# Kernel tuning notes

Hardware: AMD Instinct MI355X
Metric: run time of the kernel (lower is better)

Reference implementation:

```python
import jax, jax.numpy as jnp
import numpy as np


def setup_inputs() -> dict:
    key = jax.random.key(0)
    k1, k2 = jax.random.split(key)
    B, N, M = 4, 8192, 8192
    xyz1 = jax.random.normal(k1, (B, N, 3), dtype=jnp.float32)
    xyz2 = jax.random.normal(k2, (B, M, 3), dtype=jnp.float32)
    th = jnp.float32(0.1)
    return {"xyz1": xyz1, "xyz2": xyz2, "th": th}


def reference(xyz1, xyz2, th):
    # Pairwise squared distances (B, N, M) via the expanded form
    x2 = jnp.sum(xyz1 * xyz1, axis=-1)                    # (B, N)
    y2 = jnp.sum(xyz2 * xyz2, axis=-1)                    # (B, M)
    cross = jnp.einsum('bnd,bmd->bnm', xyz1, xyz2)        # (B, N, M)
    dist = x2[:, :, None] + y2[:, None, :] - 2.0 * cross  # (B, N, M)
    # torch: distances is (B, M, N); min over dim=1 -> per-x min (our axis=2),
    #        min over dim=2 -> per-y min (our axis=1).
    d1 = jnp.min(dist, axis=2)                            # (B, N)
    d2 = jnp.min(dist, axis=1)                            # (B, M)
    d1 = jnp.where(d1 <= th, jnp.float32(0.0), d1)
    d2 = jnp.where(d2 <= th, jnp.float32(0.0), d2)
    return jnp.mean(d1, axis=1) + jnp.mean(d2, axis=1)    # (B,)
```

## Files before the change

kernel.cpp:

```cpp
#include <hip/hip_runtime.h>
#include <math.h>

#define NPTS 8192
#define LOSCALE 2048.0f
#define INVLO   (1.0f / 2048.0f)

typedef _Float16 half8  __attribute__((ext_vector_type(8)));
typedef float    f32x16 __attribute__((ext_vector_type(16)));

__device__ __forceinline__ float min3a(float m, float a, float b) {
    float r;
    asm("v_min3_f32 %0, %1, %2, %3" : "=v"(r) : "v"(m), "v"(a), "v"(b));
    return r;
}


__global__ __launch_bounds__(256) void prep_bfrag(
    const float* __restrict__ xyz1,
    const float* __restrict__ xyz2,
    half8* __restrict__ bfrag)
{
    const int gid  = blockIdx.x * 256 + threadIdx.x;
    const int col  = gid & 31;
    const int tile = (gid >> 5) & 255;
    const int c    = gid >> 13;
    const int s    = c >> 2, bb = c & 3;
    const float* src = (s == 0 ? xyz1 : xyz2)
                     + ((size_t)bb * NPTS + tile * 32 + col) * 3;
    const float px = src[0], py = src[1], pz = src[2];
    const _Float16 phx = (_Float16)px, phy = (_Float16)py, phz = (_Float16)pz;
    const _Float16 plx = (_Float16)((px - (float)phx) * LOSCALE);
    const _Float16 ply = (_Float16)((py - (float)phy) * LOSCALE);
    const _Float16 plz = (_Float16)((pz - (float)phz) * LOSCALE);
    const float pn = px * px + py * py + pz * pz;
    const _Float16 pnh = (_Float16)pn;
    const _Float16 pnl = (_Float16)((pn - (float)pnh) * LOSCALE);
    const _Float16 one = (_Float16)1.0f, z = (_Float16)0.0f;
    half8 hi = (half8){phx, phy, phz, one, pnh, z, z, z};
    half8 lo = (half8){phx, phy, phz, plx, ply, plz, one, pnl};
    half8* dst = bfrag + ((size_t)(c * 256 + tile) * 2) * 32 + col;
    dst[0]  = hi;
    dst[32] = lo;
}

__global__ __launch_bounds__(512, 2) void chamfer_mfma(
    const float* __restrict__ xyz1,
    const float* __restrict__ xyz2,
    const half8* __restrict__ bfrag,
    const float* __restrict__ thp,
    double* __restrict__ partial)
{
    __shared__ float  red[8][4][32];
    __shared__ double wsum[8];

    const int bid    = blockIdx.x;
    const int qchunk = bid & 31;
    const int combo  = bid >> 5;
    const int b      = combo & 3;
    const int dir    = combo >> 2;
    const float* Q   = (dir == 0 ? xyz1 : xyz2) + (size_t)b * NPTS * 3;
    const int   cref = (dir == 0 ? 4 : 0) + b;

    const int lane = threadIdx.x & 63;
    const int w    = threadIdx.x >> 6;
    const int h    = lane >> 5;
    const int col  = lane & 31;
    const int qg   = w >> 2;
    const int pq   = w & 3;

    const _Float16 one = (_Float16)1.0f, z16 = (_Float16)0.0f;
    const half8 zfrag = (half8){z16, z16, z16, z16, z16, z16, z16, z16};

    half8 Ah[4], Al[4];
    f32x16 m[4];
    #pragma unroll
    for (int lt = 0; lt < 4; ++lt) {
        const float* qp = Q + ((size_t)qchunk * 256 + (qg * 4 + lt) * 32 + col) * 3;
        const float qx = qp[0], qy = qp[1], qz = qp[2];
        const float ax = -2.0f * qx, ay = -2.0f * qy, az = -2.0f * qz;
        const _Float16 ahx = (_Float16)ax, ahy = (_Float16)ay, ahz = (_Float16)az;
        const _Float16 alx = (_Float16)((ax - (float)ahx) * LOSCALE);
        const _Float16 aly = (_Float16)((ay - (float)ahy) * LOSCALE);
        const _Float16 alz = (_Float16)((az - (float)ahz) * LOSCALE);
        const float qn = qx * qx + qy * qy + qz * qz;
        const _Float16 qnh = (_Float16)qn;
        const _Float16 qnl = (_Float16)((qn - (float)qnh) * LOSCALE);
        if (h == 0) {
            Ah[lt] = (half8){ahx, ahy, ahz, qnh, one, z16, z16, z16};
            Al[lt] = (half8){alx, aly, alz, ahx, ahy, ahz, qnl, one};
        } else {
            Ah[lt] = zfrag;
            Al[lt] = zfrag;
        }
        #pragma unroll
        for (int i = 0; i < 16; ++i) m[lt][i] = INFINITY;
    }

    f32x16 zc;
    #pragma unroll
    for (int i = 0; i < 16; ++i) zc[i] = 0.0f;

    const half8* bf = bfrag + (size_t)cref * 256 * 2 * 32 + col;
    const int t0 = pq * 64;

    half8 Bh0 = zfrag, Bl0 = zfrag, Bh1 = zfrag, Bl1 = zfrag;
    if (h == 0) {
        Bh0 = bf[((size_t)(t0 + 0) * 2 + 0) * 32];
        Bl0 = bf[((size_t)(t0 + 0) * 2 + 1) * 32];
        Bh1 = bf[((size_t)(t0 + 1) * 2 + 0) * 32];
        Bl1 = bf[((size_t)(t0 + 1) * 2 + 1) * 32];
    }

    #pragma unroll 1
    for (int jp = 0; jp < 32; ++jp) {
        half8 nh0 = Bh0, nl0 = Bl0, nh1 = Bh1, nl1 = Bl1;
        if (jp < 31 && h == 0) {
            const int tn = t0 + 2 * jp + 2;
            nh0 = bf[((size_t)(tn + 0) * 2 + 0) * 32];
            nl0 = bf[((size_t)(tn + 0) * 2 + 1) * 32];
            nh1 = bf[((size_t)(tn + 1) * 2 + 0) * 32];
            nl1 = bf[((size_t)(tn + 1) * 2 + 1) * 32];
        }
        #pragma unroll
        for (int lt = 0; lt < 4; ++lt) {
            f32x16 D1 = __builtin_amdgcn_mfma_f32_32x32x16_f16(Ah[lt], Bh0, zc, 0, 0, 0);
            f32x16 D2 = __builtin_amdgcn_mfma_f32_32x32x16_f16(Al[lt], Bl0, zc, 0, 0, 0);
            f32x16 E1 = __builtin_amdgcn_mfma_f32_32x32x16_f16(Ah[lt], Bh1, zc, 0, 0, 0);
            f32x16 E2 = __builtin_amdgcn_mfma_f32_32x32x16_f16(Al[lt], Bl1, zc, 0, 0, 0);
            #pragma unroll
            for (int i = 0; i < 16; ++i) {
                const float dA = fmaf(D2[i], INVLO, D1[i]);
                const float dB = fmaf(E2[i], INVLO, E1[i]);
                m[lt][i] = min3a(m[lt][i], dA, dB);
            }
        }
        Bh0 = nh0; Bl0 = nl0; Bh1 = nh1; Bl1 = nl1;
    }

    #pragma unroll
    for (int lt = 0; lt < 4; ++lt) {
        #pragma unroll
        for (int i = 0; i < 16; ++i) {
            float v = m[lt][i];
            v = fminf(v, __shfl_xor(v, 1, 64));
            v = fminf(v, __shfl_xor(v, 2, 64));
            v = fminf(v, __shfl_xor(v, 4, 64));
            v = fminf(v, __shfl_xor(v, 8, 64));
            v = fminf(v, __shfl_xor(v, 16, 64));
            m[lt][i] = v;
        }
    }
    if (col == 0) {
        #pragma unroll
        for (int lt = 0; lt < 4; ++lt)
            #pragma unroll
            for (int i = 0; i < 16; ++i)
                red[w][lt][(i & 3) + 8 * (i >> 2) + 4 * h] = m[lt][i];
    }
    __syncthreads();

    double val = 0.0;
    if (threadIdx.x < 256) {
        const int gt  = threadIdx.x >> 5;
        const int r   = threadIdx.x & 31;
        const int qg2 = gt >> 2, lt = gt & 3;
        float mv =            red[qg2 * 4 + 0][lt][r];
        mv = fminf(mv, red[qg2 * 4 + 1][lt][r]);
        mv = fminf(mv, red[qg2 * 4 + 2][lt][r]);
        mv = fminf(mv, red[qg2 * 4 + 3][lt][r]);
        val = (mv <= *thp) ? 0.0 : (double)mv;
    }
    for (int off = 32; off > 0; off >>= 1)
        val += __shfl_down(val, off, 64);
    if (lane == 0) wsum[w] = val;
    __syncthreads();
    if (threadIdx.x == 0) {
        double s = 0.0;
        #pragma unroll
        for (int i = 0; i < 8; ++i) s += wsum[i];
        partial[bid] = s;
    }
}

__global__ __launch_bounds__(256) void chamfer_fin(
    const double* __restrict__ partial,
    float* __restrict__ out)
{
    const int b = threadIdx.x >> 6;
    const int l = threadIdx.x & 63;
    double v = (l < 32) ? partial[b * 32 + l]
                        : partial[(4 + b) * 32 + (l - 32)];
    for (int off = 32; off > 0; off >>= 1)
        v += __shfl_down(v, off, 64);
    if (l == 0) out[b] = (float)(v / (double)NPTS);
}

extern "C" void kernel_launch(void* const* d_in, const int* in_sizes, int n_in,
                              void* d_out, int out_size, void* d_ws, size_t ws_size,
                              hipStream_t stream) {
    const float* xyz1 = (const float*)d_in[0];
    const float* xyz2 = (const float*)d_in[1];
    const float* thp  = (const float*)d_in[2];
    float* out        = (float*)d_out;

    half8*  bfrag   = (half8*)d_ws;
    double* partial = (double*)((char*)d_ws + (size_t)8 * 256 * 2 * 32 * 16);

    prep_bfrag<<<256, 256, 0, stream>>>(xyz1, xyz2, bfrag);
    chamfer_mfma<<<256, 512, 0, stream>>>(xyz1, xyz2, bfrag, thp, partial);
    chamfer_fin<<<1, 256, 0, stream>>>(partial, out);
}
```

Before: 51.19 us.

## Chain hi/lo split MFMAs into accumulating pair and re-split work across blocks

Repacks the fp16 hi/lo split so the correction terms ride in the unused upper K slots of the first fragment, then chains the two MFMAs through the accumulator instead of computing two separate products and combining them with FMAs. This removes the per-element fmaf combine step from the inner loop. Work is redistributed to 512 blocks of 128 queries, with each wave scanning 32 reference tiles instead of 64. The fragments now fill both halves of the wave, so loads are unconditional, and the prep buffer doubles in size. The 64x scale factor changes the rounding behaviour of the split and may affect precision.

```diff
diff --git a/kernel.cpp b/kernel.cpp
--- a/kernel.cpp
+++ b/kernel.cpp
@@ -2,8 +2,6 @@
 #include <math.h>
 
 #define NPTS 8192
-#define LOSCALE 2048.0f
-#define INVLO   (1.0f / 2048.0f)
 
 typedef _Float16 half8  __attribute__((ext_vector_type(8)));
 typedef float    f32x16 __attribute__((ext_vector_type(16)));
@@ -21,26 +19,35 @@
     half8* __restrict__ bfrag)
 {
     const int gid  = blockIdx.x * 256 + threadIdx.x;
-    const int col  = gid & 31;
-    const int tile = (gid >> 5) & 255;
-    const int c    = gid >> 13;
+    const int lane = gid & 63;
+    const int tile = (gid >> 6) & 255;
+    const int c    = gid >> 14;
     const int s    = c >> 2, bb = c & 3;
-    const float* src = (s == 0 ? xyz1 : xyz2)
-                     + ((size_t)bb * NPTS + tile * 32 + col) * 3;
-    const float px = src[0], py = src[1], pz = src[2];
-    const _Float16 phx = (_Float16)px, phy = (_Float16)py, phz = (_Float16)pz;
-    const _Float16 plx = (_Float16)((px - (float)phx) * LOSCALE);
-    const _Float16 ply = (_Float16)((py - (float)phy) * LOSCALE);
-    const _Float16 plz = (_Float16)((pz - (float)phz) * LOSCALE);
-    const float pn = px * px + py * py + pz * pz;
-    const _Float16 pnh = (_Float16)pn;
-    const _Float16 pnl = (_Float16)((pn - (float)pnh) * LOSCALE);
-    const _Float16 one = (_Float16)1.0f, z = (_Float16)0.0f;
-    half8 hi = (half8){phx, phy, phz, one, pnh, z, z, z};
-    half8 lo = (half8){phx, phy, phz, plx, ply, plz, one, pnl};
-    half8* dst = bfrag + ((size_t)(c * 256 + tile) * 2) * 32 + col;
-    dst[0]  = hi;
-    dst[32] = lo;
+    const int col  = lane & 31, h = lane >> 5;
+
+    half8 B1 = {}, B2 = {};
+    if (h == 0) {
+        const float* src = (s == 0 ? xyz1 : xyz2)
+                         + ((size_t)bb * NPTS + tile * 32 + col) * 3;
+        const float px = src[0], py = src[1], pz = src[2];
+        const _Float16 phx = (_Float16)px, phy = (_Float16)py, phz = (_Float16)pz;
+        const _Float16 pl64x = (_Float16)((px - (float)phx) * 64.0f);
+        const _Float16 pl64y = (_Float16)((py - (float)phy) * 64.0f);
+        const _Float16 pl64z = (_Float16)((pz - (float)phz) * 64.0f);
+        const _Float16 ph64x = (_Float16)((float)phx * (1.0f / 64.0f));
+        const _Float16 ph64y = (_Float16)((float)phy * (1.0f / 64.0f));
+        const _Float16 ph64z = (_Float16)((float)phz * (1.0f / 64.0f));
+        const float pn = px * px + py * py + pz * pz;
+        const _Float16 pnh = (_Float16)pn;
+        const _Float16 pnl64 = (_Float16)((pn - (float)pnh) * 64.0f);
+        const _Float16 one = (_Float16)1.0f, i64 = (_Float16)(1.0f / 64.0f);
+        const _Float16 z = (_Float16)0.0f;
+        B1 = (half8){phx, phy, phz, one, pnh, ph64x, ph64y, ph64z};
+        B2 = (half8){pl64x, pl64y, pl64z, i64, pnl64, z, z, z};
+    }
+    half8* dst = bfrag + ((size_t)(c * 256 + tile) * 2) * 64 + lane;
+    dst[0]  = B1;
+    dst[64] = B2;
 }
 
 __global__ __launch_bounds__(512, 2) void chamfer_mfma(
@@ -54,8 +61,8 @@
     __shared__ double wsum[8];
 
     const int bid    = blockIdx.x;
-    const int qchunk = bid & 31;
-    const int combo  = bid >> 5;
+    const int qchunk = bid & 63;
+    const int combo  = bid >> 6;
     const int b      = combo & 3;
     const int dir    = combo >> 2;
     const float* Q   = (dir == 0 ? xyz1 : xyz2) + (size_t)b * NPTS * 3;
@@ -65,32 +72,31 @@
     const int w    = threadIdx.x >> 6;
     const int h    = lane >> 5;
     const int col  = lane & 31;
-    const int qg   = w >> 2;
-    const int pq   = w & 3;
-
-    const _Float16 one = (_Float16)1.0f, z16 = (_Float16)0.0f;
-    const half8 zfrag = (half8){z16, z16, z16, z16, z16, z16, z16, z16};
-
-    half8 Ah[4], Al[4];
+
+    half8 A1[4], A2[4];
     f32x16 m[4];
     #pragma unroll
     for (int lt = 0; lt < 4; ++lt) {
-        const float* qp = Q + ((size_t)qchunk * 256 + (qg * 4 + lt) * 32 + col) * 3;
-        const float qx = qp[0], qy = qp[1], qz = qp[2];
-        const float ax = -2.0f * qx, ay = -2.0f * qy, az = -2.0f * qz;
-        const _Float16 ahx = (_Float16)ax, ahy = (_Float16)ay, ahz = (_Float16)az;
-        const _Float16 alx = (_Float16)((ax - (float)ahx) * LOSCALE);
-        const _Float16 aly = (_Float16)((ay - (float)ahy) * LOSCALE);
-        const _Float16 alz = (_Float16)((az - (float)ahz) * LOSCALE);
-        const float qn = qx * qx + qy * qy + qz * qz;
-        const _Float16 qnh = (_Float16)qn;
-        const _Float16 qnl = (_Float16)((qn - (float)qnh) * LOSCALE);
+        A1[lt] = (half8){};
+        A2[lt] = (half8){};
         if (h == 0) {
-            Ah[lt] = (half8){ahx, ahy, ahz, qnh, one, z16, z16, z16};
-            Al[lt] = (half8){alx, aly, alz, ahx, ahy, ahz, qnl, one};
-        } else {
-            Ah[lt] = zfrag;
-            Al[lt] = zfrag;
+            const float* qp = Q + ((size_t)qchunk * 128 + lt * 32 + col) * 3;
+            const float qx = qp[0], qy = qp[1], qz = qp[2];
+            const float ax = -2.0f * qx, ay = -2.0f * qy, az = -2.0f * qz;
+            const _Float16 ahx = (_Float16)ax, ahy = (_Float16)ay, ahz = (_Float16)az;
+            const _Float16 al64x = (_Float16)((ax - (float)ahx) * 64.0f);
+            const _Float16 al64y = (_Float16)((ay - (float)ahy) * 64.0f);
+            const _Float16 al64z = (_Float16)((az - (float)ahz) * 64.0f);
+            const _Float16 ah64x = (_Float16)((float)ahx * (1.0f / 64.0f));
+            const _Float16 ah64y = (_Float16)((float)ahy * (1.0f / 64.0f));
+            const _Float16 ah64z = (_Float16)((float)ahz * (1.0f / 64.0f));
+            const float qn = qx * qx + qy * qy + qz * qz;
+            const _Float16 qnh = (_Float16)qn;
+            const _Float16 qnl64 = (_Float16)((qn - (float)qnh) * 64.0f);
+            const _Float16 one = (_Float16)1.0f, i64 = (_Float16)(1.0f / 64.0f);
+            const _Float16 z16 = (_Float16)0.0f;
+            A1[lt] = (half8){ahx, ahy, ahz, qnh, one, al64x, al64y, al64z};
+            A2[lt] = (half8){ah64x, ah64y, ah64z, qnl64, i64, z16, z16, z16};
         }
         #pragma unroll
         for (int i = 0; i < 16; ++i) m[lt][i] = INFINITY;
@@ -100,42 +106,30 @@
     #pragma unroll
     for (int i = 0; i < 16; ++i) zc[i] = 0.0f;
 
-    const half8* bf = bfrag + (size_t)cref * 256 * 2 * 32 + col;
-    const int t0 = pq * 64;
-
-    half8 Bh0 = zfrag, Bl0 = zfrag, Bh1 = zfrag, Bl1 = zfrag;
-    if (h == 0) {
-        Bh0 = bf[((size_t)(t0 + 0) * 2 + 0) * 32];
-        Bl0 = bf[((size_t)(t0 + 0) * 2 + 1) * 32];
-        Bh1 = bf[((size_t)(t0 + 1) * 2 + 0) * 32];
-        Bl1 = bf[((size_t)(t0 + 1) * 2 + 1) * 32];
-    }
-
+    const half8* bf = bfrag + (size_t)cref * (256 * 2 * 64) + lane;
+    const int t0 = w * 32;
+
+#define LD(t, f) bf[(size_t)(((t0 + ((t) & 31)) * 2 + (f))) * 64]
+
+    half8 h0 = LD(0, 0), l0 = LD(0, 1);
+    half8 h1 = LD(1, 0), l1 = LD(1, 1);
     #pragma unroll 1
-    for (int jp = 0; jp < 32; ++jp) {
-        half8 nh0 = Bh0, nl0 = Bl0, nh1 = Bh1, nl1 = Bl1;
-        if (jp < 31 && h == 0) {
-            const int tn = t0 + 2 * jp + 2;
-            nh0 = bf[((size_t)(tn + 0) * 2 + 0) * 32];
-            nl0 = bf[((size_t)(tn + 0) * 2 + 1) * 32];
-            nh1 = bf[((size_t)(tn + 1) * 2 + 0) * 32];
-            nl1 = bf[((size_t)(tn + 1) * 2 + 1) * 32];
+    for (int jp = 0; jp < 16; ++jp) {
+        half8 nh0 = LD(2 * jp + 2, 0), nl0 = LD(2 * jp + 2, 1);
+        half8 nh1 = LD(2 * jp + 3, 0), nl1 = LD(2 * jp + 3, 1);
+        #pragma unroll
+        for (int lt = 0; lt < 4; ++lt) {
+            f32x16 D = __builtin_amdgcn_mfma_f32_32x32x16_f16(A1[lt], h0, zc, 0, 0, 0);
+            D = __builtin_amdgcn_mfma_f32_32x32x16_f16(A2[lt], l0, D, 0, 0, 0);
+            f32x16 E = __builtin_amdgcn_mfma_f32_32x32x16_f16(A1[lt], h1, zc, 0, 0, 0);
+            E = __builtin_amdgcn_mfma_f32_32x32x16_f16(A2[lt], l1, E, 0, 0, 0);
+            #pragma unroll
+            for (int i = 0; i < 16; ++i)
+                m[lt][i] = min3a(m[lt][i], D[i], E[i]);
         }
-        #pragma unroll
-        for (int lt = 0; lt < 4; ++lt) {
-            f32x16 D1 = __builtin_amdgcn_mfma_f32_32x32x16_f16(Ah[lt], Bh0, zc, 0, 0, 0);
-            f32x16 D2 = __builtin_amdgcn_mfma_f32_32x32x16_f16(Al[lt], Bl0, zc, 0, 0, 0);
-            f32x16 E1 = __builtin_amdgcn_mfma_f32_32x32x16_f16(Ah[lt], Bh1, zc, 0, 0, 0);
-            f32x16 E2 = __builtin_amdgcn_mfma_f32_32x32x16_f16(Al[lt], Bl1, zc, 0, 0, 0);
-            #pragma unroll
-            for (int i = 0; i < 16; ++i) {
-                const float dA = fmaf(D2[i], INVLO, D1[i]);
-                const float dB = fmaf(E2[i], INVLO, E1[i]);
-                m[lt][i] = min3a(m[lt][i], dA, dB);
-            }
-        }
-        Bh0 = nh0; Bl0 = nl0; Bh1 = nh1; Bl1 = nl1;
-    }
+        h0 = nh0; l0 = nl0; h1 = nh1; l1 = nl1;
+    }
+#undef LD
 
     #pragma unroll
     for (int lt = 0; lt < 4; ++lt) {
@@ -160,14 +154,12 @@
     __syncthreads();
 
     double val = 0.0;
-    if (threadIdx.x < 256) {
-        const int gt  = threadIdx.x >> 5;
-        const int r   = threadIdx.x & 31;
-        const int qg2 = gt >> 2, lt = gt & 3;
-        float mv =            red[qg2 * 4 + 0][lt][r];
-        mv = fminf(mv, red[qg2 * 4 + 1][lt][r]);
-        mv = fminf(mv, red[qg2 * 4 + 2][lt][r]);
-        mv = fminf(mv, red[qg2 * 4 + 3][lt][r]);
+    if (threadIdx.x < 128) {
+        const int lt = threadIdx.x >> 5;
+        const int r  = threadIdx.x & 31;
+        float mv = red[0][lt][r];
+        #pragma unroll
+        for (int ww = 1; ww < 8; ++ww) mv = fminf(mv, red[ww][lt][r]);
         val = (mv <= *thp) ? 0.0 : (double)mv;
     }
     for (int off = 32; off > 0; off >>= 1)
@@ -188,8 +180,7 @@
 {
     const int b = threadIdx.x >> 6;
     const int l = threadIdx.x & 63;
-    double v = (l < 32) ? partial[b * 32 + l]
-                        : partial[(4 + b) * 32 + (l - 32)];
+    double v = partial[b * 64 + l] + partial[(4 + b) * 64 + l];
     for (int off = 32; off > 0; off >>= 1)
         v += __shfl_down(v, off, 64);
     if (l == 0) out[b] = (float)(v / (double)NPTS);
@@ -204,9 +195,9 @@
     float* out        = (float*)d_out;
 
     half8*  bfrag   = (half8*)d_ws;
-    double* partial = (double*)((char*)d_ws + (size_t)8 * 256 * 2 * 32 * 16);
-
-    prep_bfrag<<<256, 256, 0, stream>>>(xyz1, xyz2, bfrag);
-    chamfer_mfma<<<256, 512, 0, stream>>>(xyz1, xyz2, bfrag, thp, partial);
+    double* partial = (double*)((char*)d_ws + (size_t)8 * 256 * 2 * 64 * 16);
+
+    prep_bfrag<<<512, 256, 0, stream>>>(xyz1, xyz2, bfrag);
+    chamfer_mfma<<<512, 512, 0, stream>>>(xyz1, xyz2, bfrag, thp, partial);
     chamfer_fin<<<1, 256, 0, stream>>>(partial, out);
 }
```

Result: slower. 55.48 us (+8.4%).
